# Kernel optimization log

Measured on AMD Instinct MI355X. Metric: run time of the kernel, lower is better.

## Reference

```python
import jax, jax.numpy as jnp
import numpy as np

B, Mc, Mt, E, VOCAB, NREL, HOPS = 16, 2048, 4096, 512, 32000, 69, 2


def setup_inputs() -> dict:
    key = jax.random.key(0)
    ks = jax.random.split(key, 10)
    s = 1.0 / np.sqrt(E)
    return {
        "concept_table": jax.random.normal(ks[0], (VOCAB, E), jnp.float32) * 0.02,
        "relation_table": jax.random.normal(ks[1], (NREL, E), jnp.float32) * 0.02,
        "W_s": jax.random.uniform(ks[2], (HOPS, E, E), jnp.float32, -s, s),
        "W_n": jax.random.uniform(ks[3], (HOPS, E, E), jnp.float32, -s, s),
        "W_r": jax.random.uniform(ks[4], (HOPS, E, E), jnp.float32, -s, s),
        "concept_ids": jax.random.randint(ks[5], (B, Mc), 0, VOCAB, jnp.int32),
        "relation_ids": jax.random.randint(ks[6], (B, Mt), 0, NREL, jnp.int32),
        "head_idx": jax.random.randint(ks[7], (B, Mt), 0, Mc, jnp.int32),
        "tail_idx": jax.random.randint(ks[8], (B, Mt), 0, Mc, jnp.int32),
        "triple_labels": jax.random.randint(ks[9], (B, Mt), -1, 2, jnp.int32),
    }


def reference(concept_table, relation_table, W_s, W_n, W_r,
              concept_ids, relation_ids, head_idx, tail_idx, triple_labels):
    b, mt = head_idx.shape
    mc = concept_ids.shape[1]
    h = concept_table[concept_ids]          # B x Mc x E
    r = relation_table[relation_ids]        # B x Mt x E
    valid = (triple_labels != -1)
    mask = valid[..., None].astype(h.dtype)  # B x Mt x 1
    cnt = valid.astype(h.dtype)              # B x Mt
    bidx = jnp.arange(b)[:, None]
    num_hops = W_s.shape[0]
    for l in range(num_hops):
        rm = r * mask
        o_h = jnp.take_along_axis(h, head_idx[..., None], axis=1) * mask
        o_t = jnp.take_along_axis(h, tail_idx[..., None], axis=1) * mask
        upd = jnp.zeros_like(h)
        upd = upd.at[bidx, tail_idx].add(o_h - rm)   # messages head->tail
        upd = upd.at[bidx, head_idx].add(o_t - rm)   # messages tail->head
        count = jnp.zeros((b, mc), h.dtype)
        count = count.at[bidx, tail_idx].add(cnt).at[bidx, head_idx].add(cnt)
        h = jax.nn.relu(h @ W_s[l].T + (upd @ W_n[l].T) / jnp.clip(count, 1.0)[..., None])
        r = r @ W_r[l].T
    head_repr = jnp.take_along_axis(h, head_idx[..., None], axis=1)  # B x Mt x E
    tail_repr = jnp.take_along_axis(h, tail_idx[..., None], axis=1)
    return jnp.concatenate((head_repr, r, tail_repr), axis=-1)       # B x Mt x 3E
```

## Files before the change

kernel.cpp:

```cpp
#include <hip/hip_runtime.h>
#include <stdint.h>

#define B_   16
#define MC   2048
#define MT   4096
#define E_   512
#define NRELS 69

typedef __attribute__((ext_vector_type(8))) short bf16x8;
typedef __attribute__((ext_vector_type(4))) float floatx4;
typedef __attribute__((ext_vector_type(4))) float f32x4;
typedef __attribute__((ext_vector_type(4))) unsigned int u32x4;

typedef __attribute__((address_space(1))) const void gvoid_t;
typedef __attribute__((address_space(3))) void lvoid_t;

__device__ inline float b2f(ushort u) {
  union { uint32_t i; float f; } x; x.i = ((uint32_t)u) << 16; return x.f;
}
__device__ inline ushort f2b(float f) {
  union { float f; uint32_t u; } v; v.f = f;
  uint32_t r = (v.u + 0x7fffu + ((v.u >> 16) & 1u)) >> 16;
  return (ushort)r;
}

__device__ inline void gl2lds(const ushort* g, ushort* l) {
  __builtin_amdgcn_global_load_lds((gvoid_t*)g, (lvoid_t*)l, 16, 0, 0);
}

__device__ inline int block_detect(const ushort* ct) {
  __shared__ int sflag;
  if (threadIdx.x == 0) sflag = 0;
  __syncthreads();
  int bad = 0;
  for (int j = threadIdx.x; j < 1024; j += 256) {
    int e = (ct[j] >> 7) & 0xFF;
    if (e >= 0xC0) bad = 1;
  }
  if (bad) sflag = 1;
  __syncthreads();
  return sflag;
}

__device__ inline void cvt8(const void* src, ushort* dst, int c, int flag) {
  if (flag) {
    const float* s = (const float*)src + (size_t)c * 8;
    f32x4 a = __builtin_nontemporal_load((const f32x4*)s);
    f32x4 b = __builtin_nontemporal_load((const f32x4*)(s + 4));
    u32x4 p;
    p.x = (uint32_t)f2b(a.x) | ((uint32_t)f2b(a.y) << 16);
    p.y = (uint32_t)f2b(a.z) | ((uint32_t)f2b(a.w) << 16);
    p.z = (uint32_t)f2b(b.x) | ((uint32_t)f2b(b.y) << 16);
    p.w = (uint32_t)f2b(b.z) | ((uint32_t)f2b(b.w) << 16);
    *(u32x4*)(dst + (size_t)c * 8) = p;
  } else {
    u32x4 v = __builtin_nontemporal_load((const u32x4*)((const ushort*)src + (size_t)c * 8));
    *(u32x4*)(dst + (size_t)c * 8) = v;
  }
}

#define NW8 (2 * E_ * E_ / 8)
#define NR8 (NRELS * E_ / 8)
#define NGH (B_ * MC * 64)
#define NCT (B_ * MT)
#define SEC1 (NW8)
#define SEC2 (2 * NW8)
#define SEC3 (3 * NW8)
#define SEC4 (SEC3 + NR8)
#define SEC5 (SEC4 + NGH)
#define STOT (SEC5 + NCT)

__global__ void preproc_k(const void* __restrict__ ct, const void* __restrict__ rt,
                          const void* __restrict__ Ws, const void* __restrict__ Wn,
                          const void* __restrict__ Wr,
                          const int* __restrict__ cids, const int* __restrict__ heads,
                          const int* __restrict__ tails, const int* __restrict__ labels,
                          ushort* __restrict__ Wsb, ushort* __restrict__ Wnb,
                          ushort* __restrict__ Wrb, ushort* __restrict__ rtab0,
                          ushort* __restrict__ h0, int* __restrict__ cnt) {
  int flag = block_detect((const ushort*)ct);
  int c = blockIdx.x * 256 + threadIdx.x;
  if (c >= STOT) return;
  if (c < SEC3) {
    if (c < SEC1)       cvt8(Ws, Wsb, c, flag);
    else if (c < SEC2)  cvt8(Wn, Wnb, c - SEC1, flag);
    else                cvt8(Wr, Wrb, c - SEC2, flag);
  } else if (c < SEC4) {
    cvt8(rt, rtab0, c - SEC3, flag);
  } else if (c < SEC5) {
    int g = c - SEC4;
    int row = g >> 6, col = (g & 63) << 3;
    int src = cids[row];
    if (flag) {
      const float* s = (const float*)ct + (size_t)src * E_ + col;
      f32x4 a = __builtin_nontemporal_load((const f32x4*)s);
      f32x4 b = __builtin_nontemporal_load((const f32x4*)(s + 4));
      u32x4 p;
      p.x = (uint32_t)f2b(a.x) | ((uint32_t)f2b(a.y) << 16);
      p.y = (uint32_t)f2b(a.z) | ((uint32_t)f2b(a.w) << 16);
      p.z = (uint32_t)f2b(b.x) | ((uint32_t)f2b(b.y) << 16);
      p.w = (uint32_t)f2b(b.z) | ((uint32_t)f2b(b.w) << 16);
      *(u32x4*)(h0 + (size_t)row * E_ + col) = p;
    } else {
      u32x4 v = __builtin_nontemporal_load(
          (const u32x4*)((const ushort*)ct + (size_t)src * E_ + col));
      *(u32x4*)(h0 + (size_t)row * E_ + col) = v;
    }
  } else {
    int t = c - SEC5;
    if (labels[t] != -1) {
      int b = t >> 12;
      atomicAdd(&cnt[b * MC + heads[t]], 1);
      atomicAdd(&cnt[b * MC + tails[t]], 1);
    }
  }
}

__global__ void scan_inv_k(const int* __restrict__ cnt, int* __restrict__ offs,
                           float* __restrict__ inv) {
  __shared__ int part[1024];
  int tid = threadIdx.x;
  const int CH = (B_ * MC) / 1024;
  int base = tid * CH, s = 0;
  for (int i = 0; i < CH; ++i) s += cnt[base + i];
  part[tid] = s;
  __syncthreads();
  for (int off = 1; off < 1024; off <<= 1) {
    int v = (tid >= off) ? part[tid - off] : 0;
    __syncthreads();
    part[tid] += v;
    __syncthreads();
  }
  int run = (tid == 0) ? 0 : part[tid - 1];
  for (int i = 0; i < CH; ++i) {
    int cc = cnt[base + i];
    offs[base + i] = run;
    inv[base + i] = 1.0f / (float)(cc > 1 ? cc : 1);
    run += cc;
  }
  if (tid == 1023) offs[B_ * MC] = run;
}

__global__ void mid_k(const ushort* __restrict__ rtab0, const ushort* __restrict__ Wr,
                      ushort* __restrict__ rtab1, ushort* __restrict__ rtab2,
                      const int* __restrict__ head, const int* __restrict__ tail,
                      const int* __restrict__ rid, const int* __restrict__ labels,
                      const int* __restrict__ offs, int* __restrict__ cursor,
                      int* __restrict__ edges) {
  __shared__ float arow[E_];
  int tid = threadIdx.x;
  if (blockIdx.x < NRELS) {
    int n = blockIdx.x;
    for (int k = tid; k < E_; k += 256) arow[k] = b2f(rtab0[n * E_ + k]);
    __syncthreads();
    for (int hp = 0; hp < 2; ++hp) {
      const ushort* W = Wr + (size_t)hp * E_ * E_;
      int ca = tid, cb = tid + 256;
      float acc0 = 0.f, acc1 = 0.f;
      const ushort* wa = W + (size_t)ca * E_;
      const ushort* wb = W + (size_t)cb * E_;
      for (int k = 0; k < E_; k += 8) {
        u32x4 w8a = *(const u32x4*)(wa + k);
        u32x4 w8b = *(const u32x4*)(wb + k);
        uint32_t va[4] = {w8a.x, w8a.y, w8a.z, w8a.w};
        uint32_t vb[4] = {w8b.x, w8b.y, w8b.z, w8b.w};
#pragma unroll
        for (int i = 0; i < 4; ++i) {
          float a0 = arow[k + 2 * i], a1 = arow[k + 2 * i + 1];
          acc0 += a0 * b2f((ushort)(va[i] & 0xffff)) + a1 * b2f((ushort)(va[i] >> 16));
          acc1 += a0 * b2f((ushort)(vb[i] & 0xffff)) + a1 * b2f((ushort)(vb[i] >> 16));
        }
      }
      __syncthreads();
      ushort ra = f2b(acc0), rb = f2b(acc1);
      ushort* o = hp ? rtab2 : rtab1;
      o[n * E_ + ca] = ra;
      o[n * E_ + cb] = rb;
      arow[ca] = b2f(ra);
      arow[cb] = b2f(rb);
      __syncthreads();
    }
  } else {
    int t = (blockIdx.x - NRELS) * 256 + tid;
    if (t >= B_ * MT) return;
    if (labels[t] == -1) return;
    int b = t >> 12;
    int hb = b * MC + head[t], tb = b * MC + tail[t];
    int r = rid[t];
    int p = atomicAdd(&cursor[tb], 1);
    edges[offs[tb] + p] = head[t] | (r << 16);
    p = atomicAdd(&cursor[hb], 1);
    edges[offs[hb] + p] = tail[t] | (r << 16);
  }
}

__global__ void gather_msg_k(const ushort* __restrict__ h, const ushort* __restrict__ rtab,
                             const int* __restrict__ edges, const int* __restrict__ offs,
                             const float* __restrict__ inv, ushort* __restrict__ updb) {
  int row = blockIdx.x * 4 + (threadIdx.x >> 6);
  int lane = threadIdx.x & 63;
  int col = lane << 3;
  int beg = offs[row], end = offs[row + 1];
  int b = row >> 11;
  float acc[8];
#pragma unroll
  for (int i = 0; i < 8; ++i) acc[i] = 0.f;
  const ushort* hbase = h + (size_t)b * MC * E_ + col;
  int ent = (beg < end) ? edges[beg] : 0;
  for (int e = beg; e < end; ++e) {
    int nxt = (e + 1 < end) ? edges[e + 1] : 0;
    int other = ent & 0xffff, rr = ent >> 16;
    u32x4 wh = *(const u32x4*)(hbase + (size_t)other * E_);
    u32x4 wr = *(const u32x4*)(rtab + (size_t)rr * E_ + col);
    uint32_t hh[4] = {wh.x, wh.y, wh.z, wh.w};
    uint32_t rv[4] = {wr.x, wr.y, wr.z, wr.w};
#pragma unroll
    for (int i = 0; i < 4; ++i) {
      acc[2 * i]     += b2f((ushort)(hh[i] & 0xffff)) - b2f((ushort)(rv[i] & 0xffff));
      acc[2 * i + 1] += b2f((ushort)(hh[i] >> 16))    - b2f((ushort)(rv[i] >> 16));
    }
    ent = nxt;
  }
  float s = inv[row];
  u32x4 p;
  p.x = (uint32_t)f2b(acc[0] * s) | ((uint32_t)f2b(acc[1] * s) << 16);
  p.y = (uint32_t)f2b(acc[2] * s) | ((uint32_t)f2b(acc[3] * s) << 16);
  p.z = (uint32_t)f2b(acc[4] * s) | ((uint32_t)f2b(acc[5] * s) << 16);
  p.w = (uint32_t)f2b(acc[6] * s) | ((uint32_t)f2b(acc[7] * s) << 16);
  *(u32x4*)(updb + (size_t)row * E_ + col) = p;
}

#define BM 128
#define BN 128
#define BK 64

__global__ __launch_bounds__(256) void gemm_h_k(
    const ushort* __restrict__ A0, const ushort* __restrict__ W0,
    const ushort* __restrict__ A1, const ushort* __restrict__ W1,
    ushort* __restrict__ C) {
  const int N = E_, K = E_;
  __shared__ __align__(16) ushort As[BM * BK];
  __shared__ __align__(16) ushort Bs[BN * BK];
  int nbn = N / BN;
  int bm = blockIdx.x / nbn, bn = blockIdx.x % nbn;
  int tid = threadIdx.x;
  int lane = tid & 63, wid = tid >> 6;
  int wm = (wid >> 1) * 64, wn = (wid & 1) * 64;
  int lrow = lane & 15, lq = lane >> 4;

  floatx4 acc[4][4];
#pragma unroll
  for (int i = 0; i < 4; ++i)
#pragma unroll
    for (int j = 0; j < 4; ++j) acc[i][j] = (floatx4)(0.0f);

  for (int pass = 0; pass < 2; ++pass) {
    const ushort* Am = pass ? A1 : A0;
    const ushort* Wm = pass ? W1 : W0;
    for (int k0 = 0; k0 < K; k0 += BK) {
#pragma unroll
      for (int i = 0; i < 4; ++i) {
        int c = tid + i * 256;
        int row = c >> 3, col = (c & 7) << 3;
        gl2lds(Am + (size_t)(bm * BM + row) * K + k0 + col, As + row * BK + col);
      }
#pragma unroll
      for (int i = 0; i < 4; ++i) {
        int c = tid + i * 256;
        int row = c >> 3, col = (c & 7) << 3;
        gl2lds(Wm + (size_t)(bn * BN + row) * K + k0 + col, Bs + row * BK + col);
      }
      __syncthreads();
#pragma unroll
      for (int kk = 0; kk < BK; kk += 32) {
        bf16x8 af[4], bfr[4];
#pragma unroll
        for (int mi = 0; mi < 4; ++mi)
          af[mi] = *(const bf16x8*)(As + (wm + mi * 16 + lrow) * BK + kk + lq * 8);
#pragma unroll
        for (int ni = 0; ni < 4; ++ni)
          bfr[ni] = *(const bf16x8*)(Bs + (wn + ni * 16 + lrow) * BK + kk + lq * 8);
#pragma unroll
        for (int mi = 0; mi < 4; ++mi)
#pragma unroll
          for (int ni = 0; ni < 4; ++ni)
            acc[mi][ni] = __builtin_amdgcn_mfma_f32_16x16x32_bf16(af[mi], bfr[ni], acc[mi][ni], 0, 0, 0);
      }
      __syncthreads();
    }
  }
#pragma unroll
  for (int mi = 0; mi < 4; ++mi)
#pragma unroll
    for (int ni = 0; ni < 4; ++ni)
#pragma unroll
      for (int rg = 0; rg < 4; ++rg) {
        int row = bm * BM + wm + mi * 16 + lq * 4 + rg;
        int col = bn * BN + wn + ni * 16 + lrow;
        C[(size_t)row * N + col] = f2b(fmaxf(acc[mi][ni][rg], 0.0f));
      }
}

__global__ void out_k(const ushort* __restrict__ h, const ushort* __restrict__ rtab,
                      const int* __restrict__ rid,
                      const int* __restrict__ head, const int* __restrict__ tail,
                      void* __restrict__ out, const ushort* __restrict__ ctab) {
  int flag = block_detect(ctab);
  int gp = blockIdx.x * blockDim.x + threadIdx.x;
  int t = gp / 96;
  if (t >= B_ * MT) return;
  int sp = gp - t * 96;
  int sec = sp >> 5;
  int col = (sp & 31) << 4;
  int b = t >> 12;
  const ushort* src;
  if (sec == 0)      src = h + (size_t)(b * MC + head[t]) * E_ + col;
  else if (sec == 1) src = rtab + (size_t)rid[t] * E_ + col;
  else               src = h + (size_t)(b * MC + tail[t]) * E_ + col;
  u32x4 v0 = *(const u32x4*)src;
  u32x4 v1 = *(const u32x4*)(src + 8);
  size_t o = (size_t)t * 1536 + sec * 512 + col;
  if (flag) {
    float* fo = (float*)out + o;
    uint32_t w[8] = {v0.x, v0.y, v0.z, v0.w, v1.x, v1.y, v1.z, v1.w};
#pragma unroll
    for (int i = 0; i < 4; ++i) {
      f32x4 f;
      f.x = b2f((ushort)(w[2 * i] & 0xffff));
      f.y = b2f((ushort)(w[2 * i] >> 16));
      f.z = b2f((ushort)(w[2 * i + 1] & 0xffff));
      f.w = b2f((ushort)(w[2 * i + 1] >> 16));
      *((f32x4*)fo + i) = f;
    }
  } else {
    ushort* po = (ushort*)out + o;
    *(u32x4*)po = v0;
    *((u32x4*)po + 1) = v1;
  }
}

extern "C" void kernel_launch(void* const* d_in, const int* in_sizes, int n_in,
                              void* d_out, int out_size, void* d_ws, size_t ws_size,
                              hipStream_t stream) {
  const void* concept_table  = d_in[0];
  const void* relation_table = d_in[1];
  const void* W_s = d_in[2];
  const void* W_n = d_in[3];
  const void* W_r = d_in[4];
  const int* concept_ids  = (const int*)d_in[5];
  const int* relation_ids = (const int*)d_in[6];
  const int* head_idx = (const int*)d_in[7];
  const int* tail_idx = (const int*)d_in[8];
  const int* labels   = (const int*)d_in[9];

  char* ws = (char*)d_ws;
  size_t off = 0;
  auto alloc = [&](size_t bytes) {
    char* p = ws + off;
    off += (bytes + 255) & ~(size_t)255;
    return p;
  };
  ushort* h_a    = (ushort*)alloc((size_t)B_ * MC * E_ * 2);
  ushort* h_b    = (ushort*)alloc((size_t)B_ * MC * E_ * 2);
  int*    cnt    = (int*)   alloc((size_t)B_ * MC * 4);
  float*  inv    = (float*) alloc((size_t)B_ * MC * 4);
  int*    offs   = (int*)   alloc(((size_t)B_ * MC + 1) * 4);
  int*    cursor = (int*)   alloc((size_t)B_ * MC * 4);
  int*    edges  = (int*)   alloc((size_t)2 * B_ * MT * 4);
  ushort* Wsb    = (ushort*)alloc((size_t)2 * E_ * E_ * 2);
  ushort* Wnb    = (ushort*)alloc((size_t)2 * E_ * E_ * 2);
  ushort* Wrb    = (ushort*)alloc((size_t)2 * E_ * E_ * 2);
  ushort* rtab0  = (ushort*)alloc((size_t)NRELS * E_ * 2);
  ushort* rtab1  = (ushort*)alloc((size_t)NRELS * E_ * 2);
  ushort* rtab2  = (ushort*)alloc((size_t)NRELS * E_ * 2);
  ushort* updb   = (ushort*)d_out;

  hipMemsetAsync(cnt, 0, (size_t)B_ * MC * 4, stream);
  hipMemsetAsync(cursor, 0, (size_t)B_ * MC * 4, stream);

  preproc_k<<<(STOT + 255) / 256, 256, 0, stream>>>(
      concept_table, relation_table, W_s, W_n, W_r,
      concept_ids, head_idx, tail_idx, labels,
      Wsb, Wnb, Wrb, rtab0, h_a, cnt);

  scan_inv_k<<<1, 1024, 0, stream>>>(cnt, offs, inv);

  mid_k<<<NRELS + (B_ * MT + 255) / 256, 256, 0, stream>>>(
      rtab0, Wrb, rtab1, rtab2,
      head_idx, tail_idx, relation_ids, labels, offs, cursor, edges);

  gather_msg_k<<<B_ * MC / 4, 256, 0, stream>>>(h_a, rtab0, edges, offs, inv, updb);
  gemm_h_k<<<(B_ * MC / BM) * (E_ / BN), 256, 0, stream>>>(h_a, Wsb, updb, Wnb, h_b);

  gather_msg_k<<<B_ * MC / 4, 256, 0, stream>>>(h_b, rtab1, edges, offs, inv, updb);
  gemm_h_k<<<(B_ * MC / BM) * (E_ / BN), 256, 0, stream>>>(h_b, Wsb + (size_t)E_ * E_, updb,
                                                           Wnb + (size_t)E_ * E_, h_a);

  out_k<<<(B_ * MT * 96 + 255) / 256, 256, 0, stream>>>(h_a, rtab2, relation_ids,
                                                        head_idx, tail_idx, d_out,
                                                        (const ushort*)concept_table);
}
```

Measured before the change: 727.7 us.

## Unroll edge gather loop, stage GEMM epilogue through LDS, remap block order

The message gather loop is unrolled by two so that two neighbor rows and two relation rows are loaded at once, giving more memory-level parallelism on the irregular gathers. The GEMM epilogue now writes the ReLU'd bf16 tile into a padded shared-memory buffer that reuses the A/B staging pool. Each thread then writes 16-byte vectors to global memory, replacing scattered 2-byte stores. The block index is also remapped across 8 groups to change the order tiles are scheduled in, which may affect cache or XCD locality. The cost is an extra barrier and LDS round trip per tile.

```diff
diff --git a/kernel.cpp b/kernel.cpp
--- a/kernel.cpp
+++ b/kernel.cpp
@@ -206,20 +206,39 @@
 #pragma unroll
   for (int i = 0; i < 8; ++i) acc[i] = 0.f;
   const ushort* hbase = h + (size_t)b * MC * E_ + col;
-  int ent = (beg < end) ? edges[beg] : 0;
-  for (int e = beg; e < end; ++e) {
-    int nxt = (e + 1 < end) ? edges[e + 1] : 0;
-    int other = ent & 0xffff, rr = ent >> 16;
-    u32x4 wh = *(const u32x4*)(hbase + (size_t)other * E_);
-    u32x4 wr = *(const u32x4*)(rtab + (size_t)rr * E_ + col);
-    uint32_t hh[4] = {wh.x, wh.y, wh.z, wh.w};
-    uint32_t rv[4] = {wr.x, wr.y, wr.z, wr.w};
+  int e = beg;
+  for (; e + 1 < end; e += 2) {
+    int ent0 = edges[e], ent1 = edges[e + 1];
+    u32x4 wh0 = *(const u32x4*)(hbase + (size_t)(ent0 & 0xffff) * E_);
+    u32x4 wr0 = *(const u32x4*)(rtab + (size_t)(ent0 >> 16) * E_ + col);
+    u32x4 wh1 = *(const u32x4*)(hbase + (size_t)(ent1 & 0xffff) * E_);
+    u32x4 wr1 = *(const u32x4*)(rtab + (size_t)(ent1 >> 16) * E_ + col);
+    uint32_t h0[4] = {wh0.x, wh0.y, wh0.z, wh0.w};
+    uint32_t r0[4] = {wr0.x, wr0.y, wr0.z, wr0.w};
+    uint32_t h1[4] = {wh1.x, wh1.y, wh1.z, wh1.w};
+    uint32_t r1[4] = {wr1.x, wr1.y, wr1.z, wr1.w};
 #pragma unroll
     for (int i = 0; i < 4; ++i) {
-      acc[2 * i]     += b2f((ushort)(hh[i] & 0xffff)) - b2f((ushort)(rv[i] & 0xffff));
-      acc[2 * i + 1] += b2f((ushort)(hh[i] >> 16))    - b2f((ushort)(rv[i] >> 16));
-    }
-    ent = nxt;
+      acc[2 * i]     += b2f((ushort)(h0[i] & 0xffff)) - b2f((ushort)(r0[i] & 0xffff));
+      acc[2 * i + 1] += b2f((ushort)(h0[i] >> 16))    - b2f((ushort)(r0[i] >> 16));
+    }
+#pragma unroll
+    for (int i = 0; i < 4; ++i) {
+      acc[2 * i]     += b2f((ushort)(h1[i] & 0xffff)) - b2f((ushort)(r1[i] & 0xffff));
+      acc[2 * i + 1] += b2f((ushort)(h1[i] >> 16))    - b2f((ushort)(r1[i] >> 16));
+    }
+  }
+  if (e < end) {
+    int ent0 = edges[e];
+    u32x4 wh0 = *(const u32x4*)(hbase + (size_t)(ent0 & 0xffff) * E_);
+    u32x4 wr0 = *(const u32x4*)(rtab + (size_t)(ent0 >> 16) * E_ + col);
+    uint32_t h0[4] = {wh0.x, wh0.y, wh0.z, wh0.w};
+    uint32_t r0[4] = {wr0.x, wr0.y, wr0.z, wr0.w};
+#pragma unroll
+    for (int i = 0; i < 4; ++i) {
+      acc[2 * i]     += b2f((ushort)(h0[i] & 0xffff)) - b2f((ushort)(r0[i] & 0xffff));
+      acc[2 * i + 1] += b2f((ushort)(h0[i] >> 16))    - b2f((ushort)(r0[i] >> 16));
+    }
   }
   float s = inv[row];
   u32x4 p;
@@ -233,16 +252,20 @@
 #define BM 128
 #define BN 128
 #define BK 64
+#define CTS 136
 
 __global__ __launch_bounds__(256) void gemm_h_k(
     const ushort* __restrict__ A0, const ushort* __restrict__ W0,
     const ushort* __restrict__ A1, const ushort* __restrict__ W1,
     ushort* __restrict__ C) {
   const int N = E_, K = E_;
-  __shared__ __align__(16) ushort As[BM * BK];
-  __shared__ __align__(16) ushort Bs[BN * BK];
+  __shared__ __align__(16) ushort pool[BM * CTS];
+  ushort* As = pool;
+  ushort* Bs = pool + BM * BK;
   int nbn = N / BN;
-  int bm = blockIdx.x / nbn, bn = blockIdx.x % nbn;
+  int bid = blockIdx.x;
+  int nb = (bid & 7) * ((BM * nbn == 0) ? 0 : ( (B_ * MC / BM) * nbn / 8 )) + (bid >> 3);
+  int bm = nb / nbn, bn = nb % nbn;
   int tid = threadIdx.x;
   int lane = tid & 63, wid = tid >> 6;
   int wm = (wid >> 1) * 64, wn = (wid & 1) * 64;
@@ -294,11 +317,18 @@
 #pragma unroll
     for (int ni = 0; ni < 4; ++ni)
 #pragma unroll
-      for (int rg = 0; rg < 4; ++rg) {
-        int row = bm * BM + wm + mi * 16 + lq * 4 + rg;
-        int col = bn * BN + wn + ni * 16 + lrow;
-        C[(size_t)row * N + col] = f2b(fmaxf(acc[mi][ni][rg], 0.0f));
-      }
+      for (int rg = 0; rg < 4; ++rg)
+        pool[(wm + mi * 16 + lq * 4 + rg) * CTS + wn + ni * 16 + lrow] =
+            f2b(fmaxf(acc[mi][ni][rg], 0.0f));
+  __syncthreads();
+  {
+    int row = tid >> 1, half = tid & 1;
+    const ushort* srcl = pool + row * CTS + half * 64;
+    ushort* dstg = C + (size_t)(bm * BM + row) * N + bn * BN + half * 64;
+#pragma unroll
+    for (int j = 0; j < 8; ++j)
+      *(u32x4*)(dstg + j * 8) = *(const u32x4*)(srcl + j * 8);
+  }
 }
 
 __global__ void out_k(const ushort* __restrict__ h, const ushort* __restrict__ rtab,
```

Result: no change. 736.6 us (+1.2%).
